# Performance work log

Hardware: AMD Instinct MI355X
Metric: run time of the kernel (lower is better)

Reference implementation:

```python
import jax, jax.numpy as jnp
import numpy as np

B = 1
N_HEADS = 8
SEQ = 4096
HEAD_DIM = 128
BLOCK = 64          # sparse_block_size == kernel_block_size
LOCAL_BLOCKS = 16
VERT_STRIDE = 8


def _token_mask():
    """Local + vertical-strided block-sparse causal mask, per head.

    Block (qb, kb) is active for head h iff qb >= kb and
    (qb - kb < LOCAL_BLOCKS  or  (kb + h*head_step + 1) % VERT_STRIDE == 0),
    then expanded to token level and AND-ed with the token causal mask.
    """
    nb = SEQ // BLOCK
    qb = jnp.arange(nb)[:, None]                      # [nb, 1]
    kb = jnp.arange(nb)[None, :]                      # [1, nb]
    head_step = max(1, VERT_STRIDE // N_HEADS)        # hetero heads (homo_head=False)
    h = jnp.arange(N_HEADS)[:, None, None]            # [H, 1, 1]
    vert = (kb[None] + h * head_step + 1) % VERT_STRIDE == 0   # [H, 1, nb] -> broadcast
    local = (qb - kb >= 0) & (qb - kb < LOCAL_BLOCKS)          # [nb, nb]
    bmask = (qb >= kb)[None] & (local[None] | vert)            # [H, nb, nb]
    # expand block mask to token level
    tmask = jnp.repeat(jnp.repeat(bmask, BLOCK, axis=1), BLOCK, axis=2)  # [H, S, S]
    causal = jnp.arange(SEQ)[:, None] >= jnp.arange(SEQ)[None, :]
    return tmask & causal[None]


def setup_inputs() -> dict:
    key = jax.random.key(0)
    kq, kk, kv = jax.random.split(key, 3)
    q = jax.random.normal(kq, (B, N_HEADS, SEQ, HEAD_DIM), jnp.float32)
    k = jax.random.normal(kk, (B, N_HEADS, SEQ, HEAD_DIM), jnp.float32)
    v = jax.random.normal(kv, (B, N_HEADS, SEQ, HEAD_DIM), jnp.float32)
    sm_scale = jnp.float32(1.0 / np.sqrt(HEAD_DIM))
    return {"q": q, "k": k, "v": v, "sm_scale": sm_scale}


def reference(q, k, v, sm_scale):
    mask = _token_mask()                                       # [H, S, S] bool
    scores = jnp.einsum('bhqd,bhkd->bhqk', q, k) * sm_scale    # [B, H, S, S]
    neg = jnp.asarray(jnp.finfo(scores.dtype).min, scores.dtype)
    scores = jnp.where(mask[None], scores, neg)
    p = jax.nn.softmax(scores, axis=-1)
    return jnp.einsum('bhqk,bhkd->bhqd', p, v)
```

## Files before the change

kernel.cpp:

```cpp
#include <hip/hip_runtime.h>
#include <hip/hip_bf16.h>

#define HH 8
#define SEQL 4096
#define DD 128
#define NBLK 64
#define LOCAL_B 16
#define MBIAS 12.0f
#define EP_STR 132

typedef __attribute__((ext_vector_type(8))) short bf16x8;
typedef __attribute__((ext_vector_type(4))) float f32x4;
typedef unsigned short ushort_t;

typedef const __attribute__((address_space(1))) unsigned int gu32;
typedef __attribute__((address_space(3))) unsigned int lu32;

__device__ __forceinline__ unsigned short f2bf(float x) {
    union { float f; unsigned u; } a; a.f = x;
    unsigned r = a.u + 0x7FFFu + ((a.u >> 16) & 1u);
    return (unsigned short)(r >> 16);
}

__device__ __forceinline__ unsigned cvtpk_bf16(float lo, float hi) {
    unsigned r;
    asm("v_cvt_pk_bf16_f32 %0, %1, %2" : "=v"(r) : "v"(lo), "v"(hi));
    return r;
}

__device__ __forceinline__ void gload16(const void* src, void* ldsdst) {
    __builtin_amdgcn_global_load_lds((gu32*)src, (lu32*)ldsdst, 16, 0, 0);
}

#define T_STR 136
__global__ void prep(const float* __restrict__ k, const float* __restrict__ v,
                     ushort_t* __restrict__ kb, ushort_t* __restrict__ vt) {
    __shared__ ushort_t t[64 * T_STR];
    int bid = blockIdx.x;
    int tid = threadIdx.x;
    if (bid < 2048) {
        int idx = (bid * 256 + tid) * 8;
        const float4* s = (const float4*)(k + idx);
        float4 a = s[0], b = s[1];
        union { bf16x8 v8; ushort_t u[8]; } p;
        p.u[0] = f2bf(a.x); p.u[1] = f2bf(a.y); p.u[2] = f2bf(a.z); p.u[3] = f2bf(a.w);
        p.u[4] = f2bf(b.x); p.u[5] = f2bf(b.y); p.u[6] = f2bf(b.z); p.u[7] = f2bf(b.w);
        *(bf16x8*)(kb + idx) = p.v8;
        return;
    }
    int g = bid - 2048;
    int h  = g >> 6;
    int sb = g & 63;
    const float* vp = v + ((size_t)h * SEQL + sb * 64) * DD;
    {
        int col = (tid & 15) * 8;
        #pragma unroll
        for (int it = 0; it < 4; ++it) {
            int row = it * 16 + (tid >> 4);
            const float4* s = (const float4*)(vp + row * DD + col);
            float4 a = s[0], b = s[1];
            union { bf16x8 v8; ushort_t u[8]; } p;
            p.u[0] = f2bf(a.x); p.u[1] = f2bf(a.y); p.u[2] = f2bf(a.z); p.u[3] = f2bf(a.w);
            p.u[4] = f2bf(b.x); p.u[5] = f2bf(b.y); p.u[6] = f2bf(b.z); p.u[7] = f2bf(b.w);
            *(bf16x8*)&t[row * T_STR + col] = p.v8;
        }
    }
    __syncthreads();
    {
        int d = tid >> 1, seg = tid & 1;
        ushort_t* dst = vt + ((size_t)h * DD + d) * SEQL + sb * 64 + seg * 32;
        #pragma unroll
        for (int i = 0; i < 4; ++i) {
            union { bf16x8 v8; ushort_t u[8]; } o;
            #pragma unroll
            for (int e = 0; e < 8; ++e)
                o.u[e] = t[(seg * 32 + i * 8 + e) * T_STR + d];
            *(bf16x8*)(dst + i * 8) = o.v8;
        }
    }
}

__global__ __launch_bounds__(512, 4)
void bsattn8(const float* __restrict__ q, const ushort_t* __restrict__ kbuf,
             const ushort_t* __restrict__ vtbuf, const float* __restrict__ scl,
             float* __restrict__ out) {
    const int g  = blockIdx.x;
    const int h  = g & 7;
    const int i0 = g >> 3;
    const int qb = (i0 < 32) ? (63 - i0) : (i0 - 32);
    const int tid = threadIdx.x;
    const int w  = tid >> 6;
    const int wq = w & 3;
    const int kg = w >> 2;
    const int l  = tid & 63;
    const int lr = l & 15;
    const int lg = l >> 4;

    __shared__ char smem[65536];

    const float kappa = scl[0] * 1.44269504088896f;

    const float*    qh = q     + (size_t)h * SEQL * DD;
    const ushort_t* kh = kbuf  + (size_t)h * SEQL * DD;
    const ushort_t* vh = vtbuf + (size_t)h * DD * SEQL;
    float*          oh = out   + (size_t)h * SEQL * DD;

    bf16x8 qf[4];
    {
        const float* qrow = qh + (size_t)(qb * 64 + 16 * wq + lr) * DD;
        #pragma unroll
        for (int ks = 0; ks < 4; ++ks) {
            const float4* p4 = (const float4*)(qrow + ks * 32 + lg * 8);
            float4 x = p4[0], y = p4[1];
            union { bf16x8 v8; ushort_t u[8]; } pk;
            pk.u[0] = f2bf(x.x * kappa); pk.u[1] = f2bf(x.y * kappa);
            pk.u[2] = f2bf(x.z * kappa); pk.u[3] = f2bf(x.w * kappa);
            pk.u[4] = f2bf(y.x * kappa); pk.u[5] = f2bf(y.y * kappa);
            pk.u[6] = f2bf(y.z * kappa); pk.u[7] = f2bf(y.w * kappa);
            qf[ks] = pk.v8;
        }
    }

    f32x4 oacc[8];
    #pragma unroll
    for (int i = 0; i < 8; ++i) oacc[i] = (f32x4){0.f, 0.f, 0.f, 0.f};
    float lrun = 0.f;

    unsigned kA = (unsigned)(kg * 8192 + lr * 256) + (unsigned)((lg * 16) ^ ((lr & 7) << 4));
    unsigned kB = kA ^ 64u;
    unsigned vA = 32768u + (unsigned)(lr * 128) + (unsigned)(((kg * 64) + lg * 16) ^ ((lr & 7) << 4));
    unsigned kst = 0, vst = 0;

    auto stage = [&](int kb) {
        const char* kbase = (const char*)(kh + (size_t)kb * 64 * DD);
        #pragma unroll
        for (int j = 0; j < 2; ++j) {
            int row = j * 32 + w * 4 + (l >> 4);
            int col = (l & 15) * 16;
            gload16(kbase + row * 256 + (col ^ ((row & 7) << 4)),
                    smem + kst + j * 8192 + w * 1024);
        }
        const char* vbase = (const char*)vh + (size_t)kb * 128;
        #pragma unroll
        for (int j = 0; j < 2; ++j) {
            int d = j * 64 + w * 8 + (l >> 3);
            int col = (l & 7) * 16;
            gload16(vbase + (size_t)d * (SEQL * 2) + (col ^ ((d & 7) << 4)),
                    smem + 32768 + vst + j * 8192 + w * 1024);
        }
        kst ^= 16384u; vst ^= 16384u;
    };

    const bool selA = (lg >= 2);
    const bool b1 = (lg & 1);
    const bool b2 = (lg & 2);

    auto compute = [&](bool diag) {
        f32x4 sacc[2];
        #pragma unroll
        for (int ct = 0; ct < 2; ++ct)
            sacc[ct] = (f32x4){-MBIAS, -MBIAS, -MBIAS, -MBIAS};
        __builtin_amdgcn_s_setprio(1);
        #pragma unroll
        for (int ks = 0; ks < 4; ++ks) {
            #pragma unroll
            for (int ct = 0; ct < 2; ++ct) {
                bf16x8 kf = *(const bf16x8*)(smem + ((ks & 1) ? kB : kA) +
                                             ct * 4096 + (ks >> 1) * 128);
                sacc[ct] = __builtin_amdgcn_mfma_f32_16x16x32_bf16(kf, qf[ks], sacc[ct], 0, 0, 0);
            }
        }
        __builtin_amdgcn_s_setprio(0);

        float p[2][4];
        #pragma unroll
        for (int ct = 0; ct < 2; ++ct)
            #pragma unroll
            for (int j = 0; j < 4; ++j)
                p[ct][j] = exp2f(sacc[ct][j]);
        if (diag) {
            #pragma unroll
            for (int ct = 0; ct < 2; ++ct)
                #pragma unroll
                for (int j = 0; j < 4; ++j)
                    if (kg * 32 + ct * 16 + 4 * lg + j > 16 * wq + lr) p[ct][j] = 0.f;
        }
        float rs = 0.f;
        #pragma unroll
        for (int ct = 0; ct < 2; ++ct)
            #pragma unroll
            for (int j = 0; j < 4; ++j) rs += p[ct][j];
        lrun += rs;

        unsigned e0 = cvtpk_bf16(p[0][0], p[0][1]), e1 = cvtpk_bf16(p[0][2], p[0][3]);
        unsigned o0 = cvtpk_bf16(p[1][0], p[1][1]), o1 = cvtpk_bf16(p[1][2], p[1][3]);

        union { unsigned u[4]; bf16x8 v8; } pb;
        {
            unsigned m = selA ? o0 : e0, nn = selA ? e0 : o0;
            unsigned t  = __shfl_xor((int)nn, 32);
            unsigned tp = __shfl_xor((int)nn, 48);
            unsigned m16 = __shfl_xor((int)m, 16);
            pb.u[0] = b1 ? (b2 ? m16 : tp) : (b2 ? t : m);
            pb.u[2] = b1 ? (b2 ? m : t) : (b2 ? tp : m16);
        }
        {
            unsigned m = selA ? o1 : e1, nn = selA ? e1 : o1;
            unsigned t  = __shfl_xor((int)nn, 32);
            unsigned tp = __shfl_xor((int)nn, 48);
            unsigned m16 = __shfl_xor((int)m, 16);
            pb.u[1] = b1 ? (b2 ? m16 : tp) : (b2 ? t : m);
            pb.u[3] = b1 ? (b2 ? m : t) : (b2 ? tp : m16);
        }

        __builtin_amdgcn_s_setprio(1);
        #pragma unroll
        for (int dt = 0; dt < 8; ++dt) {
            bf16x8 vf = *(const bf16x8*)(smem + vA + dt * 2048);
            oacc[dt] = __builtin_amdgcn_mfma_f32_16x16x32_bf16(vf, pb.v8, oacc[dt], 0, 0, 0);
        }
        __builtin_amdgcn_s_setprio(0);
    };

    const int vstart = (7 - h) & 7;
    int lo = qb - (LOCAL_B - 1); if (lo < 0) lo = 0;
    int kb = (vstart <= qb - LOCAL_B) ? vstart : lo;
    stage(kb);
    for (;;) {
        int kn;
        if (kb < lo) { int n = kb + 8; kn = (n <= qb - LOCAL_B) ? n : lo; }
        else if (kb < qb) kn = kb + 1;
        else kn = -1;

        if (kn >= 0) {
            stage(kn);
            asm volatile("s_waitcnt vmcnt(4)" ::: "memory");
        } else {
            asm volatile("s_waitcnt vmcnt(0)" ::: "memory");
        }
        __builtin_amdgcn_sched_barrier(0);
        __builtin_amdgcn_s_barrier();
        __builtin_amdgcn_sched_barrier(0);
        compute(kb == qb);
        __builtin_amdgcn_s_barrier();
        kA ^= 16384u; kB ^= 16384u; vA ^= 16384u;
        if (kn < 0) break;
        kb = kn;
    }

    float tot = lrun;
    tot += __shfl_xor(tot, 16);
    tot += __shfl_xor(tot, 32);

    float* ep   = (float*)smem;
    float* lsum = (float*)(smem + 33792);
    float* epw  = ep + wq * 16 * EP_STR;
    if (kg == 1) {
        #pragma unroll
        for (int dt = 0; dt < 8; ++dt)
            #pragma unroll
            for (int j = 0; j < 4; ++j)
                epw[lr * EP_STR + dt * 16 + 4 * lg + j] = oacc[dt][j];
        if (lg == 0) lsum[wq * 16 + lr] = tot;
    }
    __syncthreads();
    if (kg == 0) {
        float rcp = 1.0f / (tot + lsum[wq * 16 + lr]);
        #pragma unroll
        for (int dt = 0; dt < 8; ++dt)
            #pragma unroll
            for (int j = 0; j < 4; ++j) {
                int ix = lr * EP_STR + dt * 16 + 4 * lg + j;
                epw[ix] = (epw[ix] + oacc[dt][j]) * rcp;
            }
    }
    __syncthreads();
    {
        int qr  = tid >> 3;
        int seg = tid & 7;
        const float* rp = ep + (qr >> 4) * (16 * EP_STR) + (qr & 15) * EP_STR + seg * 16;
        float* op = oh + (size_t)(qb * 64 + qr) * DD + seg * 16;
        #pragma unroll
        for (int i = 0; i < 4; ++i)
            ((float4*)op)[i] = ((const float4*)rp)[i];
    }
}

extern "C" void kernel_launch(void* const* d_in, const int* in_sizes, int n_in,
                              void* d_out, int out_size, void* d_ws, size_t ws_size,
                              hipStream_t stream) {
    const float* q   = (const float*)d_in[0];
    const float* k   = (const float*)d_in[1];
    const float* v   = (const float*)d_in[2];
    const float* scl = (const float*)d_in[3];
    float* out = (float*)d_out;

    ushort_t* Kb = (ushort_t*)d_ws;
    ushort_t* Vt = Kb + (size_t)HH * SEQL * DD;

    prep<<<dim3(2048 + HH * 64), dim3(256), 0, stream>>>(k, v, Kb, Vt);
    bsattn8<<<dim3(HH * NBLK), dim3(512), 0, stream>>>(q, Kb, Vt, scl, out);
}
```

Before: 57.25 us.

## Split key tile across 4 waves each covering all query rows, reduce outputs

Restructures the attention kernel from 8 waves (4 query groups x 2 key halves) to 4 waves that each own 16 keys of the 64-key tile and compute all 64 query rows. K fragments are loaded once per wave and reused across four query groups, and the PV product uses 16x16x16 MFMAs so the P layout needs no cross-lane shuffles. The cost is a larger register footprint (32 output accumulators per lane) and a multi-step LDS tree reduction of partial outputs across waves in the epilogue. Block size drops to 256 threads, which lowers per-CU parallelism.

Result: slower. 61.26 us (+7.0%).

```diff
diff --git a/kernel.cpp b/kernel.cpp
--- a/kernel.cpp
+++ b/kernel.cpp
@@ -7,9 +7,9 @@
 #define NBLK 64
 #define LOCAL_B 16
 #define MBIAS 12.0f
-#define EP_STR 132
 
 typedef __attribute__((ext_vector_type(8))) short bf16x8;
+typedef __attribute__((ext_vector_type(4))) short bf16x4;
 typedef __attribute__((ext_vector_type(4))) float f32x4;
 typedef unsigned short ushort_t;
 
@@ -26,6 +26,15 @@
     unsigned r;
     asm("v_cvt_pk_bf16_f32 %0, %1, %2" : "=v"(r) : "v"(lo), "v"(hi));
     return r;
+}
+
+__device__ __forceinline__ f32x4 mfma16(bf16x4 a, bf16x4 b, f32x4 c) {
+#if __has_builtin(__builtin_amdgcn_mfma_f32_16x16x16bf16_1k)
+    return __builtin_amdgcn_mfma_f32_16x16x16bf16_1k(a, b, c, 0, 0, 0);
+#else
+    asm("v_mfma_f32_16x16x16_bf16 %0, %1, %2, %0" : "+v"(c) : "v"(a), "v"(b));
+    return c;
+#endif
 }
 
 __device__ __forceinline__ void gload16(const void* src, void* ldsdst) {
@@ -80,8 +89,8 @@
     }
 }
 
-__global__ __launch_bounds__(512, 4)
-void bsattn8(const float* __restrict__ q, const ushort_t* __restrict__ kbuf,
+__global__ __launch_bounds__(256, 2)
+void bsattn9(const float* __restrict__ q, const ushort_t* __restrict__ kbuf,
              const ushort_t* __restrict__ vtbuf, const float* __restrict__ scl,
              float* __restrict__ out) {
     const int g  = blockIdx.x;
@@ -90,8 +99,6 @@
     const int qb = (i0 < 32) ? (63 - i0) : (i0 - 32);
     const int tid = threadIdx.x;
     const int w  = tid >> 6;
-    const int wq = w & 3;
-    const int kg = w >> 2;
     const int l  = tid & 63;
     const int lr = l & 15;
     const int lg = l >> 4;
@@ -105,9 +112,10 @@
     const ushort_t* vh = vtbuf + (size_t)h * DD * SEQL;
     float*          oh = out   + (size_t)h * SEQL * DD;
 
-    bf16x8 qf[4];
-    {
-        const float* qrow = qh + (size_t)(qb * 64 + 16 * wq + lr) * DD;
+    bf16x8 qf[4][4];
+    #pragma unroll
+    for (int qg = 0; qg < 4; ++qg) {
+        const float* qrow = qh + (size_t)(qb * 64 + qg * 16 + lr) * DD;
         #pragma unroll
         for (int ks = 0; ks < 4; ++ks) {
             const float4* p4 = (const float4*)(qrow + ks * 32 + lg * 8);
@@ -117,107 +125,92 @@
             pk.u[2] = f2bf(x.z * kappa); pk.u[3] = f2bf(x.w * kappa);
             pk.u[4] = f2bf(y.x * kappa); pk.u[5] = f2bf(y.y * kappa);
             pk.u[6] = f2bf(y.z * kappa); pk.u[7] = f2bf(y.w * kappa);
-            qf[ks] = pk.v8;
-        }
-    }
-
-    f32x4 oacc[8];
+            qf[qg][ks] = pk.v8;
+        }
+    }
+
+    f32x4 oacc[8][4];
     #pragma unroll
-    for (int i = 0; i < 8; ++i) oacc[i] = (f32x4){0.f, 0.f, 0.f, 0.f};
-    float lrun = 0.f;
-
-    unsigned kA = (unsigned)(kg * 8192 + lr * 256) + (unsigned)((lg * 16) ^ ((lr & 7) << 4));
+    for (int dt = 0; dt < 8; ++dt)
+        #pragma unroll
+        for (int qg = 0; qg < 4; ++qg) oacc[dt][qg] = (f32x4){0.f, 0.f, 0.f, 0.f};
+    float lrun[4] = {0.f, 0.f, 0.f, 0.f};
+
+    unsigned kA = (unsigned)((w * 16 + lr) * 256) + (unsigned)((lg * 16) ^ ((lr & 7) << 4));
     unsigned kB = kA ^ 64u;
-    unsigned vA = 32768u + (unsigned)(lr * 128) + (unsigned)(((kg * 64) + lg * 16) ^ ((lr & 7) << 4));
+    unsigned vA = 32768u + (unsigned)(lr * 128) +
+                  (unsigned)((((2 * w + (lg >> 1)) ^ (lr & 7)) << 4) + (lg & 1) * 8);
     unsigned kst = 0, vst = 0;
 
     auto stage = [&](int kb) {
         const char* kbase = (const char*)(kh + (size_t)kb * 64 * DD);
         #pragma unroll
-        for (int j = 0; j < 2; ++j) {
-            int row = j * 32 + w * 4 + (l >> 4);
+        for (int i = 0; i < 4; ++i) {
+            int row = w * 16 + i * 4 + (l >> 4);
             int col = (l & 15) * 16;
             gload16(kbase + row * 256 + (col ^ ((row & 7) << 4)),
-                    smem + kst + j * 8192 + w * 1024);
+                    smem + kst + w * 4096 + i * 1024 + l * 16);
         }
         const char* vbase = (const char*)vh + (size_t)kb * 128;
         #pragma unroll
-        for (int j = 0; j < 2; ++j) {
-            int d = j * 64 + w * 8 + (l >> 3);
-            int col = (l & 7) * 16;
-            gload16(vbase + (size_t)d * (SEQL * 2) + (col ^ ((d & 7) << 4)),
-                    smem + 32768 + vst + j * 8192 + w * 1024);
+        for (int i = 0; i < 4; ++i) {
+            int d = w * 32 + i * 8 + (l >> 3);
+            int c = (l & 7) * 16;
+            gload16(vbase + (size_t)d * (SEQL * 2) + (c ^ ((d & 7) << 4)),
+                    smem + 32768 + vst + w * 4096 + i * 1024 + l * 16);
         }
         kst ^= 16384u; vst ^= 16384u;
     };
 
-    const bool selA = (lg >= 2);
-    const bool b1 = (lg & 1);
-    const bool b2 = (lg & 2);
-
     auto compute = [&](bool diag) {
-        f32x4 sacc[2];
-        #pragma unroll
-        for (int ct = 0; ct < 2; ++ct)
-            sacc[ct] = (f32x4){-MBIAS, -MBIAS, -MBIAS, -MBIAS};
+        bf16x8 kf0 = *(const bf16x8*)(smem + kA);
+        bf16x8 kf1 = *(const bf16x8*)(smem + kB);
+        bf16x8 kf2 = *(const bf16x8*)(smem + kA + 128);
+        bf16x8 kf3 = *(const bf16x8*)(smem + kB + 128);
+        f32x4 sacc[4];
+        #pragma unroll
+        for (int qg = 0; qg < 4; ++qg)
+            sacc[qg] = (f32x4){-MBIAS, -MBIAS, -MBIAS, -MBIAS};
         __builtin_amdgcn_s_setprio(1);
         #pragma unroll
-        for (int ks = 0; ks < 4; ++ks) {
-            #pragma unroll
-            for (int ct = 0; ct < 2; ++ct) {
-                bf16x8 kf = *(const bf16x8*)(smem + ((ks & 1) ? kB : kA) +
-                                             ct * 4096 + (ks >> 1) * 128);
-                sacc[ct] = __builtin_amdgcn_mfma_f32_16x16x32_bf16(kf, qf[ks], sacc[ct], 0, 0, 0);
-            }
+        for (int qg = 0; qg < 4; ++qg) {
+            sacc[qg] = __builtin_amdgcn_mfma_f32_16x16x32_bf16(kf0, qf[qg][0], sacc[qg], 0, 0, 0);
+            sacc[qg] = __builtin_amdgcn_mfma_f32_16x16x32_bf16(kf1, qf[qg][1], sacc[qg], 0, 0, 0);
+            sacc[qg] = __builtin_amdgcn_mfma_f32_16x16x32_bf16(kf2, qf[qg][2], sacc[qg], 0, 0, 0);
+            sacc[qg] = __builtin_amdgcn_mfma_f32_16x16x32_bf16(kf3, qf[qg][3], sacc[qg], 0, 0, 0);
         }
         __builtin_amdgcn_s_setprio(0);
 
-        float p[2][4];
-        #pragma unroll
-        for (int ct = 0; ct < 2; ++ct)
+        float p[4][4];
+        #pragma unroll
+        for (int qg = 0; qg < 4; ++qg)
             #pragma unroll
             for (int j = 0; j < 4; ++j)
-                p[ct][j] = exp2f(sacc[ct][j]);
+                p[qg][j] = exp2f(sacc[qg][j]);
         if (diag) {
             #pragma unroll
-            for (int ct = 0; ct < 2; ++ct)
+            for (int qg = 0; qg < 4; ++qg)
                 #pragma unroll
                 for (int j = 0; j < 4; ++j)
-                    if (kg * 32 + ct * 16 + 4 * lg + j > 16 * wq + lr) p[ct][j] = 0.f;
-        }
-        float rs = 0.f;
-        #pragma unroll
-        for (int ct = 0; ct < 2; ++ct)
-            #pragma unroll
-            for (int j = 0; j < 4; ++j) rs += p[ct][j];
-        lrun += rs;
-
-        unsigned e0 = cvtpk_bf16(p[0][0], p[0][1]), e1 = cvtpk_bf16(p[0][2], p[0][3]);
-        unsigned o0 = cvtpk_bf16(p[1][0], p[1][1]), o1 = cvtpk_bf16(p[1][2], p[1][3]);
-
-        union { unsigned u[4]; bf16x8 v8; } pb;
-        {
-            unsigned m = selA ? o0 : e0, nn = selA ? e0 : o0;
-            unsigned t  = __shfl_xor((int)nn, 32);
-            unsigned tp = __shfl_xor((int)nn, 48);
-            unsigned m16 = __shfl_xor((int)m, 16);
-            pb.u[0] = b1 ? (b2 ? m16 : tp) : (b2 ? t : m);
-            pb.u[2] = b1 ? (b2 ? m : t) : (b2 ? tp : m16);
-        }
-        {
-            unsigned m = selA ? o1 : e1, nn = selA ? e1 : o1;
-            unsigned t  = __shfl_xor((int)nn, 32);
-            unsigned tp = __shfl_xor((int)nn, 48);
-            unsigned m16 = __shfl_xor((int)m, 16);
-            pb.u[1] = b1 ? (b2 ? m16 : tp) : (b2 ? t : m);
-            pb.u[3] = b1 ? (b2 ? m : t) : (b2 ? tp : m16);
+                    if (w * 16 + 4 * lg + j > qg * 16 + lr) p[qg][j] = 0.f;
+        }
+        bf16x4 pf[4];
+        #pragma unroll
+        for (int qg = 0; qg < 4; ++qg) {
+            lrun[qg] += p[qg][0] + p[qg][1] + p[qg][2] + p[qg][3];
+            union { unsigned u[2]; bf16x4 v4; } pk;
+            pk.u[0] = cvtpk_bf16(p[qg][0], p[qg][1]);
+            pk.u[1] = cvtpk_bf16(p[qg][2], p[qg][3]);
+            pf[qg] = pk.v4;
         }
 
         __builtin_amdgcn_s_setprio(1);
         #pragma unroll
         for (int dt = 0; dt < 8; ++dt) {
-            bf16x8 vf = *(const bf16x8*)(smem + vA + dt * 2048);
-            oacc[dt] = __builtin_amdgcn_mfma_f32_16x16x32_bf16(vf, pb.v8, oacc[dt], 0, 0, 0);
+            bf16x4 vf = *(const bf16x4*)(smem + vA + dt * 2048);
+            #pragma unroll
+            for (int qg = 0; qg < 4; ++qg)
+                oacc[dt][qg] = mfma16(vf, pf[qg], oacc[dt][qg]);
         }
         __builtin_amdgcn_s_setprio(0);
     };
@@ -234,7 +227,7 @@
 
         if (kn >= 0) {
             stage(kn);
-            asm volatile("s_waitcnt vmcnt(4)" ::: "memory");
+            asm volatile("s_waitcnt vmcnt(8)" ::: "memory");
         } else {
             asm volatile("s_waitcnt vmcnt(0)" ::: "memory");
         }
@@ -248,41 +241,81 @@
         kb = kn;
     }
 
-    float tot = lrun;
-    tot += __shfl_xor(tot, 16);
-    tot += __shfl_xor(tot, 32);
-
-    float* ep   = (float*)smem;
-    float* lsum = (float*)(smem + 33792);
-    float* epw  = ep + wq * 16 * EP_STR;
-    if (kg == 1) {
+    __syncthreads();
+    #pragma unroll
+    for (int qg = 0; qg < 4; ++qg) {
+        lrun[qg] += __shfl_xor(lrun[qg], 16);
+        lrun[qg] += __shfl_xor(lrun[qg], 32);
+    }
+    float* lsumL = (float*)smem;
+    if (lg == 0) {
+        #pragma unroll
+        for (int qg = 0; qg < 4; ++qg) lsumL[w * 64 + qg * 16 + lr] = lrun[qg];
+    }
+    __syncthreads();
+    float den[4] = {0.f, 0.f, 0.f, 0.f};
+    if (w == 0) {
+        #pragma unroll
+        for (int qg = 0; qg < 4; ++qg) {
+            float s = lsumL[qg * 16 + lr] + lsumL[64 + qg * 16 + lr] +
+                      lsumL[128 + qg * 16 + lr] + lsumL[192 + qg * 16 + lr];
+            den[qg] = 1.0f / s;
+        }
+    }
+    __syncthreads();
+
+    char* mb0 = smem;
+    char* mb1 = smem + 32768;
+    auto wrbuf = [&](char* b) {
         #pragma unroll
         for (int dt = 0; dt < 8; ++dt)
             #pragma unroll
-            for (int j = 0; j < 4; ++j)
-                epw[lr * EP_STR + dt * 16 + 4 * lg + j] = oacc[dt][j];
-        if (lg == 0) lsum[wq * 16 + lr] = tot;
-    }
-    __syncthreads();
-    if (kg == 0) {
-        float rcp = 1.0f / (tot + lsum[wq * 16 + lr]);
+            for (int qg = 0; qg < 4; ++qg) {
+                int qq = qg * 16 + lr;
+                *(f32x4*)(b + qq * 512 + (((dt * 4 + lg) ^ (qq & 7)) << 4)) = oacc[dt][qg];
+            }
+    };
+    auto addbuf = [&](char* b) {
         #pragma unroll
         for (int dt = 0; dt < 8; ++dt)
             #pragma unroll
-            for (int j = 0; j < 4; ++j) {
-                int ix = lr * EP_STR + dt * 16 + 4 * lg + j;
-                epw[ix] = (epw[ix] + oacc[dt][j]) * rcp;
+            for (int qg = 0; qg < 4; ++qg) {
+                int qq = qg * 16 + lr;
+                f32x4 vv = *(const f32x4*)(b + qq * 512 + (((dt * 4 + lg) ^ (qq & 7)) << 4));
+                oacc[dt][qg][0] += vv[0]; oacc[dt][qg][1] += vv[1];
+                oacc[dt][qg][2] += vv[2]; oacc[dt][qg][3] += vv[3];
             }
+    };
+    if (w == 2) wrbuf(mb0);
+    if (w == 3) wrbuf(mb1);
+    __syncthreads();
+    if (w == 0) addbuf(mb0);
+    if (w == 1) addbuf(mb1);
+    __syncthreads();
+    if (w == 1) wrbuf(mb0);
+    __syncthreads();
+    if (w == 0) {
+        addbuf(mb0);
+        #pragma unroll
+        for (int dt = 0; dt < 8; ++dt)
+            #pragma unroll
+            for (int qg = 0; qg < 4; ++qg) {
+                oacc[dt][qg][0] *= den[qg]; oacc[dt][qg][1] *= den[qg];
+                oacc[dt][qg][2] *= den[qg]; oacc[dt][qg][3] *= den[qg];
+            }
+        wrbuf(mb0);
     }
     __syncthreads();
     {
-        int qr  = tid >> 3;
-        int seg = tid & 7;
-        const float* rp = ep + (qr >> 4) * (16 * EP_STR) + (qr & 15) * EP_STR + seg * 16;
-        float* op = oh + (size_t)(qb * 64 + qr) * DD + seg * 16;
-        #pragma unroll
-        for (int i = 0; i < 4; ++i)
-            ((float4*)op)[i] = ((const float4*)rp)[i];
+        int qq  = tid >> 2;
+        int seg = tid & 3;
+        float* op = oh + (size_t)(qb * 64 + qq) * DD + seg * 32;
+        #pragma unroll
+        for (int i = 0; i < 8; ++i) {
+            int c = seg * 8 + i;
+            f32x4 vv = *(const f32x4*)(mb0 + qq * 512 + ((c ^ (qq & 7)) << 4));
+            *(f32x4*)(op + i * 4) = vv;
+        }
     }
 }
 
@@ -299,5 +332,5 @@
     ushort_t* Vt = Kb + (size_t)HH * SEQL * DD;
 
     prep<<<dim3(2048 + HH * 64), dim3(256), 0, stream>>>(k, v, Kb, Vt);
-    bsattn8<<<dim3(HH * NBLK), dim3(512), 0, stream>>>(q, Kb, Vt, scl, out);
-}
+    bsattn9<<<dim3(HH * NBLK), dim3(256), 0, stream>>>(q, Kb, Vt, scl, out);
+}
```
